# Performance work log

Measured on AMD Instinct MI355X. Metric: run time of the kernel, lower is better.

Reference implementation:

```python
import jax, jax.numpy as jnp
import numpy as np

B, N, L = 32, 1024, 128
K, D_E, H = 3, 16, 4


def setup_inputs() -> dict:
    key = jax.random.key(0)
    ks = jax.random.split(key, 7)
    return {
        "x": jax.random.normal(ks[0], (B, N, L), jnp.float32),
        # mild scaling on embeddings/projections keeps softmax logits in a sane range
        "psi_emb": jax.random.normal(ks[1], (N, D_E), jnp.float32) * 0.3,
        "psi": jnp.float32(1.0),
        "W_q": jax.random.normal(ks[2], (D_E, H, D_E), jnp.float32) * 0.2,
        "W_k": jax.random.normal(ks[3], (D_E, H, D_E), jnp.float32) * 0.2,
        "attn_alpha": jnp.float32(0.5),
        "F_w": jax.random.normal(ks[4], (H, D_E, K + 1, L), jnp.float32) * 0.1,
        "f_b": jax.random.normal(ks[5], (H, D_E), jnp.float32),
        "head_mix": jnp.ones((H,), jnp.float32),
    }


def reference(x, psi_emb, psi, W_q, W_k, attn_alpha, F_w, f_b, head_mix):
    # x: (B, N, L)
    n = x.shape[1]
    # --- gaussian adjacency: softmax over columns of exp(-psi * ||psi_i - psi_j||^2)
    diff = psi_emb[:, None, :] - psi_emb[None, :, :]          # (N, N, d_e)
    dist2 = jnp.sum(diff * diff, axis=-1)                     # (N, N)
    A_base = jax.nn.softmax(jnp.exp(-psi * dist2), axis=1)    # (N, N)
    # --- per-head attention adjacency
    Q = jnp.einsum('nd,dhm->nhm', psi_emb, W_q)               # (N, H, d_e)
    Kt = jnp.einsum('nd,dhm->nhm', psi_emb, W_k)              # (N, H, d_e)
    scale = 1.0 / jnp.sqrt(jnp.asarray(Q.shape[-1], x.dtype))
    A_attn = jax.nn.softmax(
        jnp.einsum('nhd,mhd->hnm', Q, Kt) * scale, axis=-1)   # (H, N, N)
    # --- sigmoid blend (all heads at once)
    alpha = jax.nn.sigmoid(attn_alpha)
    A_eff = alpha * A_base[None] + (1.0 - alpha) * A_attn     # (H, N, N)
    # --- Chebyshev recursion: T0 = I, T1 = A, Tk = 2 A T_{k-1} - T_{k-2}
    I = jnp.broadcast_to(jnp.eye(n, dtype=x.dtype), A_eff.shape)
    supports = [I, A_eff]
    for _ in range(2, K + 1):
        supports.append(2.0 * jnp.einsum('hnm,hml->hnl', A_eff, supports[-1]) - supports[-2])
    S = jnp.stack(supports, axis=1)                           # (H, K+1, N, N)
    # --- per-node filters
    W_filter = jnp.einsum('nd,hdkl->hnkl', psi_emb, F_w)      # (H, N, K+1, L)
    b_filter = jnp.einsum('nd,hd->hn', psi_emb, f_b)          # (H, N)
    # --- graph conv + node-specific contraction
    x_g = jnp.einsum('hknm,bml->bhknl', S, x)                 # (B, H, K+1, N, L)
    out_h = jnp.einsum('bhknl,hnkl->bhn', x_g, W_filter) + b_filter[None]
    # --- head mixing
    mix_w = jax.nn.softmax(head_mix, axis=0)                  # (H,)
    return jnp.einsum('bhn,h->bn', out_h, mix_w)              # (B, N)
```

## Files before the change

kernel.cpp:

```cpp
#include <hip/hip_runtime.h>
#include <cstdint>

#define NN 1024
#define BB 32
#define LL 128
#define DE 16
#define HH 4
#define K1 4
#define BD 512
#define NS 524288

using bf16x8 = __attribute__((ext_vector_type(8))) short;
using f32x4  = __attribute__((ext_vector_type(4))) float;

__device__ inline unsigned short f2bf(float f) {
    unsigned u = __builtin_bit_cast(unsigned, f);
    u += 0x7FFFu + ((u >> 16) & 1u);
    return (unsigned short)(u >> 16);
}
__device__ inline float bf2f(unsigned short u) {
    return __builtin_bit_cast(float, (unsigned)u << 16);
}

struct LogitsSmem {
    float ejs[64][17];
    float eis[64][17];
    float kjs[64][64];
    float qis[4][64][17];
    float part[4][5][64];
    float wq[1024];
    float wk[1024];
};
struct XtSmem { float xs[64][128]; };

__global__ __launch_bounds__(256) void phase1(
    const float* __restrict__ psi_emb, const float* __restrict__ psi_p,
    const float* __restrict__ W_q, const float* __restrict__ W_k,
    const float* __restrict__ x, const float* __restrict__ F_w,
    short* __restrict__ bnt, short* __restrict__ ant, float* __restrict__ partials,
    short* __restrict__ xt, short* __restrict__ wtt)
{
    __shared__ __align__(16) char smem_raw[sizeof(LogitsSmem)];
    const int bid = blockIdx.x;
    const int tid = threadIdx.x;

    if (bid < 256) {
        LogitsSmem& S = *(LogitsSmem*)smem_raw;
        const int jb = bid & 15, ib = bid >> 4;
        const int i0 = ib * 64, j0 = jb * 64;
        {
            const int row = tid >> 2, dq = (tid & 3) * 4;
            const float4 vj = *(const float4*)(psi_emb + (j0 + row) * DE + dq);
            S.ejs[row][dq] = vj.x; S.ejs[row][dq + 1] = vj.y;
            S.ejs[row][dq + 2] = vj.z; S.ejs[row][dq + 3] = vj.w;
            const float4 vi = *(const float4*)(psi_emb + (i0 + row) * DE + dq);
            S.eis[row][dq] = vi.x; S.eis[row][dq + 1] = vi.y;
            S.eis[row][dq + 2] = vi.z; S.eis[row][dq + 3] = vi.w;
            *(float4*)&S.wq[tid * 4] = *(const float4*)(W_q + tid * 4);
            *(float4*)&S.wk[tid * 4] = *(const float4*)(W_k + tid * 4);
        }
        __syncthreads();
#pragma unroll
        for (int rep = 0; rep < 16; rep++) {
            const int idx = rep * 256 + tid;
            const int row = idx >> 6, hm = idx & 63;
            float qv = 0.f, kv = 0.f;
#pragma unroll
            for (int d = 0; d < DE; d++) {
                qv += S.eis[row][d] * S.wq[d * 64 + hm];
                kv += S.ejs[row][d] * S.wk[d * 64 + hm];
            }
            S.qis[hm >> 4][row][hm & 15] = qv;
            S.kjs[row][hm] = kv;
        }
        __syncthreads();

        const int i = tid & 63, jg = tid >> 6;
        const float psi = psi_p[0];
        float er[DE];
#pragma unroll
        for (int d = 0; d < DE; d++) er[d] = S.eis[i][d];

        float sb = 0.f, sa[HH] = {0.f, 0.f, 0.f, 0.f};
#pragma unroll
        for (int g = 0; g < 2; g++) {
            unsigned short bw[8];
#pragma unroll
            for (int r = 0; r < 8; r++) {
                const int j = jg * 16 + g * 8 + r;
                float d2 = 0.f;
#pragma unroll
                for (int d = 0; d < DE; d++) { const float t = er[d] - S.ejs[j][d]; d2 += t * t; }
                const float bn = __expf(__expf(-psi * d2));
                sb += bn;
                bw[r] = f2bf(bn);
            }
            uint4 pk;
            pk.x = bw[0] | ((unsigned)bw[1] << 16);
            pk.y = bw[2] | ((unsigned)bw[3] << 16);
            pk.z = bw[4] | ((unsigned)bw[5] << 16);
            pk.w = bw[6] | ((unsigned)bw[7] << 16);
            const size_t toff = (size_t)((j0 + jg * 16 + g * 8) >> 3) * 8192 + (size_t)(i0 + i) * 8;
            *(uint4*)(bnt + toff) = pk;
        }
#pragma unroll
        for (int h = 0; h < HH; h++) {
            float qr[DE];
#pragma unroll
            for (int m = 0; m < DE; m++) qr[m] = S.qis[h][i][m];
#pragma unroll
            for (int g = 0; g < 2; g++) {
                unsigned short aw[8];
#pragma unroll
                for (int r = 0; r < 8; r++) {
                    const int j = jg * 16 + g * 8 + r;
                    float dot = 0.f;
#pragma unroll
                    for (int m = 0; m < DE; m++) dot += qr[m] * S.kjs[j][h * DE + m];
                    const float an = __expf(dot * 0.25f);
                    sa[h] += an;
                    aw[r] = f2bf(an);
                }
                uint4 pk;
                pk.x = aw[0] | ((unsigned)aw[1] << 16);
                pk.y = aw[2] | ((unsigned)aw[3] << 16);
                pk.z = aw[4] | ((unsigned)aw[5] << 16);
                pk.w = aw[6] | ((unsigned)aw[7] << 16);
                const size_t toff = (size_t)((j0 + jg * 16 + g * 8) >> 3) * 8192 + (size_t)(i0 + i) * 8;
                *(uint4*)(ant + (size_t)h * 1048576 + toff) = pk;
            }
        }
        S.part[jg][0][i] = sb;
#pragma unroll
        for (int h = 0; h < HH; h++) S.part[jg][1 + h][i] = sa[h];
        __syncthreads();
        if (tid < 64) {
#pragma unroll
            for (int s = 0; s < 5; s++) {
                const float v = S.part[0][s][tid] + S.part[1][s][tid] +
                                S.part[2][s][tid] + S.part[3][s][tid];
                partials[(size_t)jb * 5120 + (size_t)s * 1024 + i0 + tid] = v;
            }
        }
    } else if (bid < 768) {
        XtSmem& X = *(XtSmem*)smem_raw;
        const int idx = bid - 256;
        const int m0 = (idx & 15) * 64;
        const int b  = idx >> 4;
        for (int i = tid; i < 2048; i += 256) {
            const int row = i >> 5, lq = i & 31;
            *(float4*)&X.xs[row][lq * 4] =
                *(const float4*)(x + ((size_t)(b * NN + m0 + row)) * LL + lq * 4);
        }
        __syncthreads();
        for (int j = tid; j < 1024; j += 256) {
            const int m = j & 63, lc = j >> 6;
            const float* s = &X.xs[m][lc * 8];
            uint4 pk;
            pk.x = f2bf(s[0]) | ((unsigned)f2bf(s[1]) << 16);
            pk.y = f2bf(s[2]) | ((unsigned)f2bf(s[3]) << 16);
            pk.z = f2bf(s[4]) | ((unsigned)f2bf(s[5]) << 16);
            pk.w = f2bf(s[6]) | ((unsigned)f2bf(s[7]) << 16);
            *(uint4*)(xt + (size_t)b * 131072 + (size_t)lc * 8192 + (size_t)(m0 + m) * 8) = pk;
        }
    } else {
        const int j = (bid - 768) * 256 + tid;
        const int lc = j >> 8, c = j & 255;
        const int h = c >> 6, k = (c >> 4) & 3, d = c & 15;
        const float* s = F_w + (size_t)((h * DE + d) * K1 + k) * LL + lc * 8;
        uint4 pk;
        pk.x = f2bf(s[0]) | ((unsigned)f2bf(s[1]) << 16);
        pk.y = f2bf(s[2]) | ((unsigned)f2bf(s[3]) << 16);
        pk.z = f2bf(s[4]) | ((unsigned)f2bf(s[5]) << 16);
        pk.w = f2bf(s[6]) | ((unsigned)f2bf(s[7]) << 16);
        *(uint4*)(wtt + (size_t)lc * 2048 + (size_t)c * 8) = pk;
    }
}

__global__ __launch_bounds__(256) void phase2(
    const short* __restrict__ xt, const short* __restrict__ wtt,
    float* __restrict__ Gs, short* __restrict__ g3t,
    const short* __restrict__ bnt, const short* __restrict__ ant,
    const float* __restrict__ partials, const float* __restrict__ alpha_p,
    short* __restrict__ At)
{
    const int bid = blockIdx.x;
    const int tid = threadIdx.x;
    __shared__ float sums_l[5][64];

    if (bid < 1024) {
        const int cb = bid & 3;
        const int m0 = ((bid >> 2) & 15) * 64;
        const int bp = bid >> 6;
        const int wave = tid >> 6, lane = tid & 63;
        const int b  = bp * 2 + (wave >> 1);
        const int wc = wave & 1;
        const int q = lane >> 4, m16 = lane & 15;
        const short* xb = xt + (size_t)b * 131072;

        f32x4 acc[4][2];
#pragma unroll
        for (int mi = 0; mi < 4; mi++)
#pragma unroll
            for (int ni = 0; ni < 2; ni++) acc[mi][ni] = (f32x4){0.f, 0.f, 0.f, 0.f};

#pragma unroll
        for (int ks = 0; ks < 4; ks++) {
            const int kc = ks * 4 + q;
            bf16x8 a[4], bb[2];
#pragma unroll
            for (int mi = 0; mi < 4; mi++)
                a[mi] = *(const bf16x8*)(xb + (size_t)kc * 8192 + (size_t)(m0 + mi * 16 + m16) * 8);
#pragma unroll
            for (int ni = 0; ni < 2; ni++)
                bb[ni] = *(const bf16x8*)(wtt + (size_t)kc * 2048 +
                                          (size_t)(cb * 64 + wc * 32 + ni * 16 + m16) * 8);
#pragma unroll
            for (int mi = 0; mi < 4; mi++)
#pragma unroll
                for (int ni = 0; ni < 2; ni++)
                    acc[mi][ni] = __builtin_amdgcn_mfma_f32_16x16x32_bf16(a[mi], bb[ni], acc[mi][ni], 0, 0, 0);
        }

#pragma unroll
        for (int ni = 0; ni < 2; ni++) {
            const int cc = cb * 64 + wc * 32 + ni * 16 + m16;
            const int kk = (cc >> 4) & 3, hh = cc >> 6;
            const int slab = kk * 4 + hh;
            const int col512 = b * 16 + (cc & 15);
            float* gdst = Gs + (size_t)slab * NS;
#pragma unroll
            for (int mi = 0; mi < 4; mi++) {
                const int row0 = m0 + mi * 16 + q * 4;
#pragma unroll
                for (int r = 0; r < 4; r++)
                    gdst[(size_t)(row0 + r) * BD + col512] = acc[mi][ni][r];
                if (kk == 3) {
                    ushort4 pk;
                    pk.x = f2bf(acc[mi][ni][0]); pk.y = f2bf(acc[mi][ni][1]);
                    pk.z = f2bf(acc[mi][ni][2]); pk.w = f2bf(acc[mi][ni][3]);
                    *(ushort4*)(g3t + (size_t)hh * 524288 +
                                ((size_t)(row0 >> 3) * 512 + col512) * 8 + (row0 & 7)) = pk;
                }
            }
        }
    } else {
        const int idx = bid - 1024;
        const int jb = idx & 15, ib = idx >> 4;
        const int i0 = ib * 64, j0 = jb * 64;
        const int lane = tid & 63, w = tid >> 6;
        {
            float acc = 0.f;
#pragma unroll
            for (int jb2 = 0; jb2 < 16; jb2++)
                acc += partials[(size_t)jb2 * 5120 + (size_t)w * 1024 + i0 + lane];
            sums_l[w][lane] = acc;
            if (w == 0) {
                float a4 = 0.f;
#pragma unroll
                for (int jb2 = 0; jb2 < 16; jb2++)
                    a4 += partials[(size_t)jb2 * 5120 + 4 * 1024 + i0 + lane];
                sums_l[4][lane] = a4;
            }
        }
        __syncthreads();
        const int i = lane, jg = w;
        const float alpha = 1.f / (1.f + __expf(-alpha_p[0]));
        const float ibs = alpha / sums_l[0][i];
        float ias[HH];
#pragma unroll
        for (int h = 0; h < HH; h++) ias[h] = (1.f - alpha) / sums_l[1 + h][i];

#pragma unroll
        for (int g = 0; g < 2; g++) {
            const size_t toff = (size_t)((j0 + jg * 16 + g * 8) >> 3) * 8192 + (size_t)(i0 + i) * 8;
            const uint4 bp = *(const uint4*)(bnt + toff);
            float bnv[8];
            bnv[0] = bf2f(bp.x & 0xFFFF); bnv[1] = bf2f(bp.x >> 16);
            bnv[2] = bf2f(bp.y & 0xFFFF); bnv[3] = bf2f(bp.y >> 16);
            bnv[4] = bf2f(bp.z & 0xFFFF); bnv[5] = bf2f(bp.z >> 16);
            bnv[6] = bf2f(bp.w & 0xFFFF); bnv[7] = bf2f(bp.w >> 16);
#pragma unroll
            for (int h = 0; h < HH; h++) {
                const uint4 ap = *(const uint4*)(ant + (size_t)h * 1048576 + toff);
                float av[8];
                av[0] = bf2f(ap.x & 0xFFFF); av[1] = bf2f(ap.x >> 16);
                av[2] = bf2f(ap.y & 0xFFFF); av[3] = bf2f(ap.y >> 16);
                av[4] = bf2f(ap.z & 0xFFFF); av[5] = bf2f(ap.z >> 16);
                av[6] = bf2f(ap.w & 0xFFFF); av[7] = bf2f(ap.w >> 16);
                unsigned short ow[8];
#pragma unroll
                for (int r = 0; r < 8; r++) ow[r] = f2bf(ibs * bnv[r] + ias[h] * av[r]);
                uint4 pk;
                pk.x = ow[0] | ((unsigned)ow[1] << 16);
                pk.y = ow[2] | ((unsigned)ow[3] << 16);
                pk.z = ow[4] | ((unsigned)ow[5] << 16);
                pk.w = ow[6] | ((unsigned)ow[7] << 16);
                *(uint4*)(At + (size_t)h * 1048576 + toff) = pk;
            }
        }
    }
}

__global__ __launch_bounds__(256) void gemm_mf(
    const short* __restrict__ At, const short* __restrict__ Bt,
    const float* __restrict__ P, const float* __restrict__ Q,
    float* __restrict__ O, short* __restrict__ Ot,
    float scale, float pc, float qc, int writeO, int writeOt)
{
    const int h = blockIdx.z;
    const short* Ah = At + (size_t)h * 1048576;
    const short* Bh = Bt + (size_t)h * 524288;
    const float* Ph = P + (size_t)h * NS;
    const float* Qh = Q + (size_t)h * NS;
    float* Oh = O + (size_t)h * NS;
    short* Oth = Ot + (size_t)h * 524288;

    const int c0 = blockIdx.x * 64;
    const int r0 = blockIdx.y * 64;
    const int tid = threadIdx.x;
    const int wave = tid >> 6, lane = tid & 63;
    const int q = lane >> 4, m16 = lane & 15;
    const int wr = wave >> 1, wc = wave & 1;

    __shared__ __align__(16) short As[2][2048];
    __shared__ __align__(16) short Bs[2][2048];

    {
        uint4 ra = *(const uint4*)(Ah + ((size_t)wave * 1024 + r0 + lane) * 8);
        uint4 rb = *(const uint4*)(Bh + ((size_t)wave * 512 + c0 + lane) * 8);
        *(uint4*)&As[0][wave * 512 + lane * 8] = ra;
        *(uint4*)&Bs[0][wave * 512 + lane * 8] = rb;
    }
    __syncthreads();

    f32x4 acc[2][2];
#pragma unroll
    for (int mi = 0; mi < 2; mi++)
#pragma unroll
        for (int ni = 0; ni < 2; ni++) acc[mi][ni] = (f32x4){0.f, 0.f, 0.f, 0.f};

    int buf = 0;
    for (int k0 = 32; k0 <= 1024; k0 += 32) {
        uint4 na, nb;
        const bool more = (k0 < 1024);
        if (more) {
            na = *(const uint4*)(Ah + (((size_t)(k0 >> 3) + wave) * 1024 + r0 + lane) * 8);
            nb = *(const uint4*)(Bh + (((size_t)(k0 >> 3) + wave) * 512 + c0 + lane) * 8);
        }
        bf16x8 af0 = *(const bf16x8*)&As[buf][q * 512 + (wr * 32 + m16) * 8];
        bf16x8 af1 = *(const bf16x8*)&As[buf][q * 512 + (wr * 32 + 16 + m16) * 8];
        bf16x8 bf0 = *(const bf16x8*)&Bs[buf][q * 512 + (wc * 32 + m16) * 8];
        bf16x8 bf1 = *(const bf16x8*)&Bs[buf][q * 512 + (wc * 32 + 16 + m16) * 8];
        acc[0][0] = __builtin_amdgcn_mfma_f32_16x16x32_bf16(af0, bf0, acc[0][0], 0, 0, 0);
        acc[0][1] = __builtin_amdgcn_mfma_f32_16x16x32_bf16(af0, bf1, acc[0][1], 0, 0, 0);
        acc[1][0] = __builtin_amdgcn_mfma_f32_16x16x32_bf16(af1, bf0, acc[1][0], 0, 0, 0);
        acc[1][1] = __builtin_amdgcn_mfma_f32_16x16x32_bf16(af1, bf1, acc[1][1], 0, 0, 0);
        if (more) {
            const int nx = buf ^ 1;
            *(uint4*)&As[nx][wave * 512 + lane * 8] = na;
            *(uint4*)&Bs[nx][wave * 512 + lane * 8] = nb;
            __syncthreads();
            buf = nx;
        }
    }

#pragma unroll
    for (int mi = 0; mi < 2; mi++) {
        const int row0 = r0 + wr * 32 + mi * 16 + q * 4;
#pragma unroll
        for (int ni = 0; ni < 2; ni++) {
            const int cc = c0 + wc * 32 + ni * 16 + m16;
            float v[4];
#pragma unroll
            for (int r = 0; r < 4; r++) {
                const size_t off = (size_t)(row0 + r) * BD + cc;
                float t = scale * acc[mi][ni][r] + pc * Ph[off];
                if (qc != 0.f) t += qc * Qh[off];
                v[r] = t;
                if (writeO) Oh[off] = t;
            }
            if (writeOt) {
                ushort4 pk;
                pk.x = f2bf(v[0]); pk.y = f2bf(v[1]); pk.z = f2bf(v[2]); pk.w = f2bf(v[3]);
                *(ushort4*)(Oth + ((size_t)(row0 >> 3) * 512 + cc) * 8 + (row0 & 7)) = pk;
            }
        }
    }
}

__global__ __launch_bounds__(256) void gemm3_out(
    const short* __restrict__ At, const short* __restrict__ Bt,
    const float* __restrict__ P, const float* __restrict__ Q,
    const float* __restrict__ psi_emb, const float* __restrict__ f_b,
    const float* __restrict__ head_mix, float* __restrict__ out)
{
    const int h = blockIdx.z;
    const short* Ah = At + (size_t)h * 1048576;
    const short* Bh = Bt + (size_t)h * 524288;
    const float* Ph = P + (size_t)h * NS;
    const float* Qh = Q + (size_t)h * NS;

    const int c0 = blockIdx.x * 64;
    const int r0 = blockIdx.y * 64;
    const int tid = threadIdx.x;
    const int wave = tid >> 6, lane = tid & 63;
    const int q = lane >> 4, m16 = lane & 15;
    const int wr = wave >> 1, wc = wave & 1;

    __shared__ __align__(16) short As[2][2048];
    __shared__ __align__(16) short Bs[2][2048];
    __shared__ float es[64][17];

    {
        uint4 ra = *(const uint4*)(Ah + ((size_t)wave * 1024 + r0 + lane) * 8);
        uint4 rb = *(const uint4*)(Bh + ((size_t)wave * 512 + c0 + lane) * 8);
        *(uint4*)&As[0][wave * 512 + lane * 8] = ra;
        *(uint4*)&Bs[0][wave * 512 + lane * 8] = rb;
        const int row = tid >> 2, dq = (tid & 3) * 4;
        const float4 ev = *(const float4*)(psi_emb + (size_t)(r0 + row) * DE + dq);
        es[row][dq] = ev.x; es[row][dq + 1] = ev.y;
        es[row][dq + 2] = ev.z; es[row][dq + 3] = ev.w;
    }
    __syncthreads();

    f32x4 acc[2][2];
#pragma unroll
    for (int mi = 0; mi < 2; mi++)
#pragma unroll
        for (int ni = 0; ni < 2; ni++) acc[mi][ni] = (f32x4){0.f, 0.f, 0.f, 0.f};

    int buf = 0;
    for (int k0 = 32; k0 <= 1024; k0 += 32) {
        uint4 na, nb;
        const bool more = (k0 < 1024);
        if (more) {
            na = *(const uint4*)(Ah + (((size_t)(k0 >> 3) + wave) * 1024 + r0 + lane) * 8);
            nb = *(const uint4*)(Bh + (((size_t)(k0 >> 3) + wave) * 512 + c0 + lane) * 8);
        }
        bf16x8 af0 = *(const bf16x8*)&As[buf][q * 512 + (wr * 32 + m16) * 8];
        bf16x8 af1 = *(const bf16x8*)&As[buf][q * 512 + (wr * 32 + 16 + m16) * 8];
        bf16x8 bf0 = *(const bf16x8*)&Bs[buf][q * 512 + (wc * 32 + m16) * 8];
        bf16x8 bf1 = *(const bf16x8*)&Bs[buf][q * 512 + (wc * 32 + 16 + m16) * 8];
        acc[0][0] = __builtin_amdgcn_mfma_f32_16x16x32_bf16(af0, bf0, acc[0][0], 0, 0, 0);
        acc[0][1] = __builtin_amdgcn_mfma_f32_16x16x32_bf16(af0, bf1, acc[0][1], 0, 0, 0);
        acc[1][0] = __builtin_amdgcn_mfma_f32_16x16x32_bf16(af1, bf0, acc[1][0], 0, 0, 0);
        acc[1][1] = __builtin_amdgcn_mfma_f32_16x16x32_bf16(af1, bf1, acc[1][1], 0, 0, 0);
        if (more) {
            const int nx = buf ^ 1;
            *(uint4*)&As[nx][wave * 512 + lane * 8] = na;
            *(uint4*)&Bs[nx][wave * 512 + lane * 8] = nb;
            __syncthreads();
            buf = nx;
        }
    }

    const float hm0 = head_mix[0], hm1 = head_mix[1], hm2 = head_mix[2], hm3 = head_mix[3];
    const float mx = fmaxf(fmaxf(hm0, hm1), fmaxf(hm2, hm3));
    const float w0 = expf(hm0 - mx), w1 = expf(hm1 - mx), w2 = expf(hm2 - mx), w3 = expf(hm3 - mx);
    const float isum = 1.f / (w0 + w1 + w2 + w3);
    const float mwh = (h == 0 ? w0 : h == 1 ? w1 : h == 2 ? w2 : w3) * isum;
    const float fb = f_b[h * DE + m16];

#pragma unroll
    for (int mi = 0; mi < 2; mi++) {
        const int rloc0 = wr * 32 + mi * 16 + q * 4;
#pragma unroll
        for (int ni = 0; ni < 2; ni++) {
            const int cc = c0 + wc * 32 + ni * 16 + m16;
            const int b = cc >> 4;
#pragma unroll
            for (int r = 0; r < 4; r++) {
                const size_t off = (size_t)(r0 + rloc0 + r) * BD + cc;
                const float v = acc[mi][ni][r] + Ph[off] - Qh[off];
                float w = es[rloc0 + r][m16] * (v + fb);
                w += __shfl_xor(w, 1, 64);
                w += __shfl_xor(w, 2, 64);
                w += __shfl_xor(w, 4, 64);
                w += __shfl_xor(w, 8, 64);
                if (m16 == 0)
                    atomicAdd(out + (size_t)b * NN + (r0 + rloc0 + r), mwh * w);
            }
        }
    }
}

extern "C" void kernel_launch(void* const* d_in, const int* in_sizes, int n_in,
                              void* d_out, int out_size, void* d_ws, size_t ws_size,
                              hipStream_t stream)
{
    const float* x          = (const float*)d_in[0];
    const float* psi_emb    = (const float*)d_in[1];
    const float* psi        = (const float*)d_in[2];
    const float* W_q        = (const float*)d_in[3];
    const float* W_k        = (const float*)d_in[4];
    const float* attn_alpha = (const float*)d_in[5];
    const float* F_w        = (const float*)d_in[6];
    const float* f_b        = (const float*)d_in[7];
    const float* head_mix   = (const float*)d_in[8];
    float* out = (float*)d_out;

    short* At  = (short*)d_ws;
    short* xt  = At + 4194304;
    short* wtt = xt + 4194304;
    short* g3t = wtt + 32768;
    short* b2t = g3t + 2097152;
    short* b1t = b2t + 2097152;
    short* bnt = b1t + 2097152;
    short* ant = bnt + 1048576;
    float* Gs  = (float*)(ant + 4194304);
    float* b2  = Gs + 16 * (size_t)NS;
    float* partials = b2 + (size_t)HH * NS;

    const size_t need_bytes =
        (size_t)(4194304 + 4194304 + 32768 + 2097152 + 2097152 + 2097152 + 1048576 + 4194304) * 2 +
        (size_t)(16 * (size_t)NS + HH * NS + 81920) * 4;
    if (ws_size < need_bytes) return;

    hipMemsetAsync(out, 0, (size_t)out_size * sizeof(float), stream);
    phase1<<<784, 256, 0, stream>>>(psi_emb, psi, W_q, W_k, x, F_w,
                                    bnt, ant, partials, xt, wtt);
    phase2<<<1280, 256, 0, stream>>>(xt, wtt, Gs, g3t, bnt, ant, partials,
                                     attn_alpha, At);

    const dim3 gg(BD / 64, NN / 64, HH);
    gemm_mf<<<gg, 256, 0, stream>>>(At, g3t, Gs + 8 * (size_t)NS, Gs + 8 * (size_t)NS,
                                    b2, b2t, 2.f, 1.f, 0.f, 1, 1);
    gemm_mf<<<gg, 256, 0, stream>>>(At, b2t, Gs + 4 * (size_t)NS, Gs + 12 * (size_t)NS,
                                    b2 , b1t, 2.f, 1.f, -1.f, 0, 1);
    gemm3_out<<<gg, 256, 0, stream>>>(At, b1t, Gs, b2, psi_emb, f_b, head_mix, out);
}
```

Before: 173.1 us.

## Store intermediate G slabs and Chebyshev residuals in bf16 tiled layout

Replaces the fp32 G slabs (16 slabs) and the fp32 b2 buffer with bf16 tiles in the same layout the MFMA B operand uses. The epilogues of the Chebyshev GEMMs now read and write bf16 instead of fp32, which roughly halves the epilogue traffic and removes the duplicate fp32/bf16 writes. The memset of the output is folded into extra phase1 blocks, saving one launch. The cost is extra bf16 rounding on the residual terms P and Q, which reduces accuracy.

```diff
diff --git a/kernel.cpp b/kernel.cpp
--- a/kernel.cpp
+++ b/kernel.cpp
@@ -38,7 +38,7 @@
     const float* __restrict__ W_q, const float* __restrict__ W_k,
     const float* __restrict__ x, const float* __restrict__ F_w,
     short* __restrict__ bnt, short* __restrict__ ant, float* __restrict__ partials,
-    short* __restrict__ xt, short* __restrict__ wtt)
+    short* __restrict__ xt, short* __restrict__ wtt, float* __restrict__ out)
 {
     __shared__ __align__(16) char smem_raw[sizeof(LogitsSmem)];
     const int bid = blockIdx.x;
@@ -163,7 +163,7 @@
             pk.w = f2bf(s[6]) | ((unsigned)f2bf(s[7]) << 16);
             *(uint4*)(xt + (size_t)b * 131072 + (size_t)lc * 8192 + (size_t)(m0 + m) * 8) = pk;
         }
-    } else {
+    } else if (bid < 784) {
         const int j = (bid - 768) * 256 + tid;
         const int lc = j >> 8, c = j & 255;
         const int h = c >> 6, k = (c >> 4) & 3, d = c & 15;
@@ -174,12 +174,17 @@
         pk.z = f2bf(s[4]) | ((unsigned)f2bf(s[5]) << 16);
         pk.w = f2bf(s[6]) | ((unsigned)f2bf(s[7]) << 16);
         *(uint4*)(wtt + (size_t)lc * 2048 + (size_t)c * 8) = pk;
+    } else {
+        const int idx = (bid - 784) * 256 + tid;
+        const float4 z = {0.f, 0.f, 0.f, 0.f};
+        *(float4*)(out + (size_t)idx * 8) = z;
+        *(float4*)(out + (size_t)idx * 8 + 4) = z;
     }
 }
 
 __global__ __launch_bounds__(256) void phase2(
     const short* __restrict__ xt, const short* __restrict__ wtt,
-    float* __restrict__ Gs, short* __restrict__ g3t,
+    short* __restrict__ Gt,
     const short* __restrict__ bnt, const short* __restrict__ ant,
     const float* __restrict__ partials, const float* __restrict__ alpha_p,
     short* __restrict__ At)
@@ -226,22 +231,15 @@
         for (int ni = 0; ni < 2; ni++) {
             const int cc = cb * 64 + wc * 32 + ni * 16 + m16;
             const int kk = (cc >> 4) & 3, hh = cc >> 6;
-            const int slab = kk * 4 + hh;
             const int col512 = b * 16 + (cc & 15);
-            float* gdst = Gs + (size_t)slab * NS;
+            short* gdst = Gt + (size_t)(kk * 4 + hh) * 524288;
 #pragma unroll
             for (int mi = 0; mi < 4; mi++) {
                 const int row0 = m0 + mi * 16 + q * 4;
-#pragma unroll
-                for (int r = 0; r < 4; r++)
-                    gdst[(size_t)(row0 + r) * BD + col512] = acc[mi][ni][r];
-                if (kk == 3) {
-                    ushort4 pk;
-                    pk.x = f2bf(acc[mi][ni][0]); pk.y = f2bf(acc[mi][ni][1]);
-                    pk.z = f2bf(acc[mi][ni][2]); pk.w = f2bf(acc[mi][ni][3]);
-                    *(ushort4*)(g3t + (size_t)hh * 524288 +
-                                ((size_t)(row0 >> 3) * 512 + col512) * 8 + (row0 & 7)) = pk;
-                }
+                ushort4 pk;
+                pk.x = f2bf(acc[mi][ni][0]); pk.y = f2bf(acc[mi][ni][1]);
+                pk.z = f2bf(acc[mi][ni][2]); pk.w = f2bf(acc[mi][ni][3]);
+                *(ushort4*)(gdst + ((size_t)(row0 >> 3) * 512 + col512) * 8 + (row0 & 7)) = pk;
             }
         }
     } else {
@@ -304,17 +302,15 @@
 
 __global__ __launch_bounds__(256) void gemm_mf(
     const short* __restrict__ At, const short* __restrict__ Bt,
-    const float* __restrict__ P, const float* __restrict__ Q,
-    float* __restrict__ O, short* __restrict__ Ot,
-    float scale, float pc, float qc, int writeO, int writeOt)
+    const short* __restrict__ Pt, const short* __restrict__ Qt,
+    short* __restrict__ Ot, float scale, float pc, float qc)
 {
     const int h = blockIdx.z;
     const short* Ah = At + (size_t)h * 1048576;
     const short* Bh = Bt + (size_t)h * 524288;
-    const float* Ph = P + (size_t)h * NS;
-    const float* Qh = Q + (size_t)h * NS;
-    float* Oh = O + (size_t)h * NS;
-    short* Oth = Ot + (size_t)h * 524288;
+    const short* Ph = Pt + (size_t)h * 524288;
+    const short* Qh = Qt + (size_t)h * 524288;
+    short* Oh = Ot + (size_t)h * 524288;
 
     const int c0 = blockIdx.x * 64;
     const int r0 = blockIdx.y * 64;
@@ -371,35 +367,36 @@
 #pragma unroll
         for (int ni = 0; ni < 2; ni++) {
             const int cc = c0 + wc * 32 + ni * 16 + m16;
+            const size_t off = ((size_t)(row0 >> 3) * 512 + cc) * 8 + (row0 & 7);
+            const ushort4 pv = *(const ushort4*)(Ph + off);
             float v[4];
-#pragma unroll
-            for (int r = 0; r < 4; r++) {
-                const size_t off = (size_t)(row0 + r) * BD + cc;
-                float t = scale * acc[mi][ni][r] + pc * Ph[off];
-                if (qc != 0.f) t += qc * Qh[off];
-                v[r] = t;
-                if (writeO) Oh[off] = t;
-            }
-            if (writeOt) {
-                ushort4 pk;
-                pk.x = f2bf(v[0]); pk.y = f2bf(v[1]); pk.z = f2bf(v[2]); pk.w = f2bf(v[3]);
-                *(ushort4*)(Oth + ((size_t)(row0 >> 3) * 512 + cc) * 8 + (row0 & 7)) = pk;
-            }
+            v[0] = scale * acc[mi][ni][0] + pc * bf2f(pv.x);
+            v[1] = scale * acc[mi][ni][1] + pc * bf2f(pv.y);
+            v[2] = scale * acc[mi][ni][2] + pc * bf2f(pv.z);
+            v[3] = scale * acc[mi][ni][3] + pc * bf2f(pv.w);
+            if (qc != 0.f) {
+                const ushort4 qv = *(const ushort4*)(Qh + off);
+                v[0] += qc * bf2f(qv.x); v[1] += qc * bf2f(qv.y);
+                v[2] += qc * bf2f(qv.z); v[3] += qc * bf2f(qv.w);
+            }
+            ushort4 pk;
+            pk.x = f2bf(v[0]); pk.y = f2bf(v[1]); pk.z = f2bf(v[2]); pk.w = f2bf(v[3]);
+            *(ushort4*)(Oh + off) = pk;
         }
     }
 }
 
 __global__ __launch_bounds__(256) void gemm3_out(
     const short* __restrict__ At, const short* __restrict__ Bt,
-    const float* __restrict__ P, const float* __restrict__ Q,
+    const short* __restrict__ Pt, const short* __restrict__ Qt,
     const float* __restrict__ psi_emb, const float* __restrict__ f_b,
     const float* __restrict__ head_mix, float* __restrict__ out)
 {
     const int h = blockIdx.z;
     const short* Ah = At + (size_t)h * 1048576;
     const short* Bh = Bt + (size_t)h * 524288;
-    const float* Ph = P + (size_t)h * NS;
-    const float* Qh = Q + (size_t)h * NS;
+    const short* Ph = Pt + (size_t)h * 524288;
+    const short* Qh = Qt + (size_t)h * 524288;
 
     const int c0 = blockIdx.x * 64;
     const int r0 = blockIdx.y * 64;
@@ -465,21 +462,28 @@
 #pragma unroll
     for (int mi = 0; mi < 2; mi++) {
         const int rloc0 = wr * 32 + mi * 16 + q * 4;
+        const int row0 = r0 + rloc0;
 #pragma unroll
         for (int ni = 0; ni < 2; ni++) {
             const int cc = c0 + wc * 32 + ni * 16 + m16;
             const int b = cc >> 4;
+            const size_t off = ((size_t)(row0 >> 3) * 512 + cc) * 8 + (row0 & 7);
+            const ushort4 pv = *(const ushort4*)(Ph + off);
+            const ushort4 qv = *(const ushort4*)(Qh + off);
+            float v[4];
+            v[0] = acc[mi][ni][0] + bf2f(pv.x) - bf2f(qv.x);
+            v[1] = acc[mi][ni][1] + bf2f(pv.y) - bf2f(qv.y);
+            v[2] = acc[mi][ni][2] + bf2f(pv.z) - bf2f(qv.z);
+            v[3] = acc[mi][ni][3] + bf2f(pv.w) - bf2f(qv.w);
 #pragma unroll
             for (int r = 0; r < 4; r++) {
-                const size_t off = (size_t)(r0 + rloc0 + r) * BD + cc;
-                const float v = acc[mi][ni][r] + Ph[off] - Qh[off];
-                float w = es[rloc0 + r][m16] * (v + fb);
+                float w = es[rloc0 + r][m16] * (v[r] + fb);
                 w += __shfl_xor(w, 1, 64);
                 w += __shfl_xor(w, 2, 64);
                 w += __shfl_xor(w, 4, 64);
                 w += __shfl_xor(w, 8, 64);
                 if (m16 == 0)
-                    atomicAdd(out + (size_t)b * NN + (r0 + rloc0 + r), mwh * w);
+                    atomicAdd(out + (size_t)b * NN + (row0 + r), mwh * w);
             }
         }
     }
@@ -503,30 +507,27 @@
     short* At  = (short*)d_ws;
     short* xt  = At + 4194304;
     short* wtt = xt + 4194304;
-    short* g3t = wtt + 32768;
-    short* b2t = g3t + 2097152;
+    short* Gt  = wtt + 32768;
+    short* b2t = Gt + 8388608;
     short* b1t = b2t + 2097152;
     short* bnt = b1t + 2097152;
     short* ant = bnt + 1048576;
-    float* Gs  = (float*)(ant + 4194304);
-    float* b2  = Gs + 16 * (size_t)NS;
-    float* partials = b2 + (size_t)HH * NS;
+    float* partials = (float*)(ant + 4194304);
 
     const size_t need_bytes =
-        (size_t)(4194304 + 4194304 + 32768 + 2097152 + 2097152 + 2097152 + 1048576 + 4194304) * 2 +
-        (size_t)(16 * (size_t)NS + HH * NS + 81920) * 4;
+        (size_t)(4194304 + 4194304 + 32768 + 8388608 + 2097152 + 2097152 + 1048576 + 4194304) * 2 +
+        (size_t)81920 * 4;
     if (ws_size < need_bytes) return;
 
-    hipMemsetAsync(out, 0, (size_t)out_size * sizeof(float), stream);
-    phase1<<<784, 256, 0, stream>>>(psi_emb, psi, W_q, W_k, x, F_w,
-                                    bnt, ant, partials, xt, wtt);
-    phase2<<<1280, 256, 0, stream>>>(xt, wtt, Gs, g3t, bnt, ant, partials,
+    phase1<<<800, 256, 0, stream>>>(psi_emb, psi, W_q, W_k, x, F_w,
+                                    bnt, ant, partials, xt, wtt, out);
+    phase2<<<1280, 256, 0, stream>>>(xt, wtt, Gt, bnt, ant, partials,
                                      attn_alpha, At);
 
     const dim3 gg(BD / 64, NN / 64, HH);
-    gemm_mf<<<gg, 256, 0, stream>>>(At, g3t, Gs + 8 * (size_t)NS, Gs + 8 * (size_t)NS,
-                                    b2, b2t, 2.f, 1.f, 0.f, 1, 1);
-    gemm_mf<<<gg, 256, 0, stream>>>(At, b2t, Gs + 4 * (size_t)NS, Gs + 12 * (size_t)NS,
-                                    b2 , b1t, 2.f, 1.f, -1.f, 0, 1);
-    gemm3_out<<<gg, 256, 0, stream>>>(At, b1t, Gs, b2, psi_emb, f_b, head_mix, out);
-}
+    gemm_mf<<<gg, 256, 0, stream>>>(At, Gt + 12 * (size_t)524288, Gt + 8 * (size_t)524288,
+                                    Gt , b2t, 2.f, 1.f, 0.f);
+    gemm_mf<<<gg, 256, 0, stream>>>(At, b2t, Gt + 4 * (size_t)524288,
+                                    Gt + 12 * (size_t)524288, b1t, 2.f, 1.f, -1.f);
+    gemm3_out<<<gg, 256, 0, stream>>>(At, b1t, Gt, b2t, psi_emb, f_b, head_mix, out);
+}
```

Result: faster. 155.9 us (-10.0%).
